# Kernel optimization log

Hardware: AMD Instinct MI355X
Metric: run time of the kernel (lower is better)

## Reference

```python
import jax, jax.numpy as jnp
import numpy as np

B, L, D, F = 1, 4096, 4096, 11008
# (start, end, side): side 0 = vision expert, side 1 = language expert.
# Mirrors merge_section_size over alternating contiguous vision/language token ranges.
SEGMENTS = [(0, 1024, 0), (1024, 2048, 1), (2048, 3072, 0), (3072, 4096, 1)]


def setup_inputs() -> dict:
    key = jax.random.key(0)
    ks = jax.random.split(key, 7)
    s = 0.02  # weight init scale
    hidden_states = jax.random.normal(ks[0], (B, L, D), jnp.float32)
    tt = np.zeros((B, L), np.int32)
    for a, b, side in SEGMENTS:
        tt[:, a:b] = side
    token_type_ids = jnp.asarray(tt)
    lg_w = jax.random.normal(ks[1], (D, F), jnp.float32) * s
    lu_w = jax.random.normal(ks[2], (D, F), jnp.float32) * s
    ld_w = jax.random.normal(ks[3], (F, D), jnp.float32) * s
    vg_w = jax.random.normal(ks[4], (D, F), jnp.float32) * s
    vu_w = jax.random.normal(ks[5], (D, F), jnp.float32) * s
    vd_w = jax.random.normal(ks[6], (F, D), jnp.float32) * s
    return {
        'hidden_states': hidden_states,
        'token_type_ids': token_type_ids,
        'lg_w': lg_w, 'lu_w': lu_w, 'ld_w': ld_w,
        'vg_w': vg_w, 'vu_w': vu_w, 'vd_w': vd_w,
    }


def _swiglu_mlp(x, gw, uw, dw):
    # x: [B, T, D] -> [B, T, D]; down(silu(gate(x)) * up(x))
    h = jax.nn.silu(jnp.einsum('btd,df->btf', x, gw)) * jnp.einsum('btd,df->btf', x, uw)
    return jnp.einsum('btf,fd->btd', h, dw)


def reference(hidden_states, token_type_ids, lg_w, lu_w, ld_w, vg_w, vu_w, vd_w):
    # Split-dispatch over static contiguous segments, then concat along seq dim.
    outs = []
    for a, b, side in SEGMENTS:
        seg = hidden_states[:, a:b, :]
        if side == 1:
            outs.append(_swiglu_mlp(seg, lg_w, lu_w, ld_w))
        else:
            outs.append(_swiglu_mlp(seg, vg_w, vu_w, vd_w))
    return jnp.concatenate(outs, axis=1)
```

## Files before the change

### kernel.cpp

```cpp
#include <hip/hip_runtime.h>
#include <math.h>

typedef unsigned short u16;
typedef short s16x8 __attribute__((ext_vector_type(8)));
typedef float f32x16 __attribute__((ext_vector_type(16)));

#define GLOAD16(gp, lp)                                                        \
  __builtin_amdgcn_global_load_lds(                                            \
      (const __attribute__((address_space(1))) void*)(gp),                     \
      (__attribute__((address_space(3))) void*)(lp), 16, 0, 0)

__device__ __forceinline__ u16 f2bf(float f) {
  union { float f; unsigned u; } v; v.f = f;
  unsigned r = v.u + 0x7fffu + ((v.u >> 16) & 1u);
  return (u16)(r >> 16);
}

__global__ __launch_bounds__(256) void cvt_x_kernel(const float* __restrict__ in,
                                                    u16* __restrict__ out) {
  size_t i = ((size_t)blockIdx.x * 256 + threadIdx.x) * 8;
  float4 a = *(const float4*)(in + i);
  float4 b = *(const float4*)(in + i + 4);
  s16x8 v;
  v[0] = (short)f2bf(a.x); v[1] = (short)f2bf(a.y);
  v[2] = (short)f2bf(a.z); v[3] = (short)f2bf(a.w);
  v[4] = (short)f2bf(b.x); v[5] = (short)f2bf(b.y);
  v[6] = (short)f2bf(b.z); v[7] = (short)f2bf(b.w);
  *(s16x8*)(out + i) = v;
}

__global__ __launch_bounds__(256) void transpose_cvt_kernel(
    const float* __restrict__ in0, const float* __restrict__ in1,
    const float* __restrict__ in2, const float* __restrict__ in3,
    const float* __restrict__ in4, const float* __restrict__ in5,
    u16* __restrict__ o01, u16* __restrict__ o23,
    u16* __restrict__ o4, u16* __restrict__ o5) {
  __shared__ float s[64 * 65];
  const int mat = blockIdx.y;
  const float* in; u16* out;
  switch (mat) {
    case 0: in = in0; out = o01; break;
    case 1: in = in1; out = o01; break;
    case 2: in = in2; out = o23; break;
    case 3: in = in3; out = o23; break;
    case 4: in = in4; out = o4; break;
    default: in = in5; out = o5; break;
  }
  const int R = (mat < 4) ? 4096 : 11008;
  const int C = (mat < 4) ? 11008 : 4096;
  const int nTc = C >> 6;
  const int tr = blockIdx.x / nTc, tc = blockIdx.x - tr * nTc;
  const int r0 = tr << 6, c0 = tc << 6;
  const int t = threadIdx.x;
#pragma unroll
  for (int p = 0; p < 4; ++p) {
    const int lr = p * 16 + (t >> 4);
    const int lc = (t & 15) * 4;
    float4 v = *(const float4*)(in + (size_t)(r0 + lr) * C + (c0 + lc));
    float* sp = &s[lr * 65 + lc];
    sp[0] = v.x; sp[1] = v.y; sp[2] = v.z; sp[3] = v.w;
  }
  __syncthreads();
#pragma unroll
  for (int q = 0; q < 2; ++q) {
    const int oc = q * 32 + (t >> 3);
    const int orr = (t & 7) * 8;
    s16x8 v;
#pragma unroll
    for (int i = 0; i < 8; ++i) v[i] = (short)f2bf(s[(orr + i) * 65 + oc]);
    const int f = c0 + oc;
    size_t orow;
    if (mat < 4) orow = (size_t)((f >> 7) << 8) + ((mat & 1) << 7) + (f & 127);
    else         orow = (size_t)f;
    *(s16x8*)(out + orow * R + (r0 + orr)) = v;
  }
}

#define SBAR() __builtin_amdgcn_s_barrier()
#define LGKM0() asm volatile("s_waitcnt lgkmcnt(0)")
#define LGKM8() asm volatile("s_waitcnt lgkmcnt(8)")
#define VMCNT6() asm volatile("s_waitcnt vmcnt(6)")
#define VMCNT0() asm volatile("s_waitcnt vmcnt(0)")

#define LDA(d, mh)                                                             \
  do {                                                                         \
    _Pragma("unroll") for (int fj = 0; fj < 2; ++fj)                           \
        _Pragma("unroll") for (int ks = 0; ks < 4; ++ks)                       \
        af[fj][ks] = *(const s16x8*)(ldsA + (d) * 32768 + (mh) * 16384 +       \
                                     arow + fj * 4096 + cx[ks]);               \
  } while (0)
#define LDB(d, nh)                                                             \
  do {                                                                         \
    _Pragma("unroll") for (int ks = 0; ks < 4; ++ks)                           \
        bf[nh][ks] = *(const s16x8*)(ldsB + (d) * 32768 + (nh) * 16384 +       \
                                     brow + cx[ks]);                           \
  } while (0)
#define MFMA8(mh, nh)                                                          \
  do {                                                                         \
    __builtin_amdgcn_s_setprio(1);                                             \
    _Pragma("unroll") for (int fj = 0; fj < 2; ++fj)                           \
        _Pragma("unroll") for (int ks = 0; ks < 4; ++ks)                       \
        acc[mh][fj][nh] = __builtin_amdgcn_mfma_f32_32x32x16_bf16(             \
            af[fj][ks], bf[nh][ks], acc[mh][fj][nh], 0, 0, 0);                 \
    __builtin_amdgcn_s_setprio(0);                                             \
  } while (0)

#define STG_A(d, h, kt)                                                        \
  do {                                                                         \
    GLOAD16(srcA + (size_t)((h) * 128) * KB + (size_t)(kt) * 128,              \
            ldsA + (d) * 32768 + (h) * 16384 + woff);                          \
    GLOAD16(srcA + (size_t)((h) * 128 + 64) * KB + (size_t)(kt) * 128,         \
            ldsA + (d) * 32768 + (h) * 16384 + 8192 + woff);                   \
  } while (0)
#define STG_B(d, h, kt)                                                        \
  do {                                                                         \
    GLOAD16(srcB + (size_t)((h) * 128) * KB + (size_t)(kt) * 128,              \
            ldsB + (d) * 32768 + (h) * 16384 + woff);                          \
    GLOAD16(srcB + (size_t)((h) * 128 + 64) * KB + (size_t)(kt) * 128,         \
            ldsB + (d) * 32768 + (h) * 16384 + 8192 + woff);                   \
  } while (0)

#define GEMM_PIPE(NKT)                                                         \
  do {                                                                         \
    STG_A(0, 0, 0); STG_B(0, 0, 0); STG_B(0, 1, 0); STG_A(0, 1, 0);            \
    STG_A(1, 0, 1); STG_B(1, 0, 1); STG_B(1, 1, 1);                            \
    VMCNT6();                                                                  \
    SBAR();                                                                    \
    for (int T = 0; T < (NKT)-2; T += 2) {                                     \
      LDA(0, 0); LDB(0, 0);                                                    \
      STG_A(1, 1, T + 1);                                                      \
      LGKM8();                                                                 \
      SBAR(); LGKM0(); MFMA8(0, 0); SBAR();                                    \
      LDB(0, 1);                                                               \
      STG_A(0, 0, T + 2);                                                      \
      SBAR(); LGKM0(); MFMA8(0, 1); SBAR();                                    \
      LDA(0, 1);                                                               \
      STG_B(0, 0, T + 2);                                                      \
      SBAR(); LGKM0(); MFMA8(1, 1); SBAR();                                    \
      STG_B(0, 1, T + 2);                                                      \
      VMCNT6();                                                                \
      SBAR(); MFMA8(1, 0); SBAR();                                             \
      LDA(1, 0); LDB(1, 0);                                                    \
      STG_A(0, 1, T + 2);                                                      \
      LGKM8();                                                                 \
      SBAR(); LGKM0(); MFMA8(0, 0); SBAR();                                    \
      LDB(1, 1);                                                               \
      STG_A(1, 0, T + 3);                                                      \
      SBAR(); LGKM0(); MFMA8(0, 1); SBAR();                                    \
      LDA(1, 1);                                                               \
      STG_B(1, 0, T + 3);                                                      \
      SBAR(); LGKM0(); MFMA8(1, 1); SBAR();                                    \
      STG_B(1, 1, T + 3);                                                      \
      VMCNT6();                                                                \
      SBAR(); MFMA8(1, 0); SBAR();                                             \
    }                                                                          \
    LDA(0, 0); LDB(0, 0);                                                      \
    STG_A(1, 1, (NKT)-1);                                                      \
    LGKM8();                                                                   \
    SBAR(); LGKM0(); MFMA8(0, 0); SBAR();                                      \
    LDB(0, 1);                                                                 \
    SBAR(); LGKM0(); MFMA8(0, 1); SBAR();                                      \
    LDA(0, 1);                                                                 \
    SBAR(); LGKM0(); MFMA8(1, 1); SBAR();                                      \
    VMCNT0();                                                                  \
    SBAR(); MFMA8(1, 0); SBAR();                                               \
    LDA(1, 0); LDB(1, 0);                                                      \
    LGKM8();                                                                   \
    SBAR(); LGKM0(); MFMA8(0, 0); SBAR();                                      \
    LDB(1, 1);                                                                 \
    SBAR(); LGKM0(); MFMA8(0, 1); SBAR();                                      \
    LDA(1, 1);                                                                 \
    SBAR(); LGKM0(); MFMA8(1, 1); SBAR();                                      \
    MFMA8(1, 0);                                                               \
  } while (0)

__global__ __launch_bounds__(512, 1) void gemm_gateup_persist(
    const u16* __restrict__ A, const u16* __restrict__ GUl,
    const u16* __restrict__ GUv, const int* __restrict__ tt,
    u16* __restrict__ H, int* __restrict__ qcnt) {
  constexpr int KB = 8192;
  __shared__ u16 sA[2][2][128][64];
  __shared__ u16 sB[2][2][128][64];
  __shared__ int sQ;

  const int t = threadIdx.x;
  const int lane = t & 63;
  const int l31 = lane & 31;
  const int kg = lane >> 5;
  const int wn = (t >> 6) & 3;
  const int wm = (t >> 8) & 1;

  const int rowq = t >> 3;
  const int gsw = ((t & 7) ^ (rowq & 7) ^ ((rowq >> 3) & 3)) << 4;
  char* ldsA = (char*)&sA[0][0][0][0];
  char* ldsB = (char*)&sB[0][0][0][0];
  const int woff = (t & 448) << 4;

  const int arow = (wm * 64 + l31) * 128;
  const int brow = (wn * 32 + l31) * 128;
  int cx[4];
#pragma unroll
  for (int ks = 0; ks < 4; ++ks)
    cx[ks] = ((2 * ks + kg) ^ (l31 & 7) ^ ((l31 >> 3) & 3)) << 4;

  for (;;) {
    __syncthreads();
    if (t == 0) sQ = atomicAdd(qcnt, 1);
    __syncthreads();
    const int q = sQ;
    if (q >= 1376) break;
    const int nT = q >> 4;
    const int mT = q & 15;
    const int side = tt[mT << 8];
    const u16* GU = side ? GUl : GUv;
    const char* srcA = (const char*)A + (size_t)(mT * 256 + rowq) * KB + gsw;
    const char* srcB = (const char*)GU + (size_t)(nT * 256 + rowq) * KB + gsw;

    s16x8 af[2][4], bf[2][4];
    f32x16 acc[2][2][2];
#pragma unroll
    for (int a = 0; a < 2; ++a)
#pragma unroll
      for (int b = 0; b < 2; ++b)
#pragma unroll
        for (int c2 = 0; c2 < 2; ++c2)
#pragma unroll
          for (int r = 0; r < 16; ++r) acc[a][b][c2][r] = 0.f;

    GEMM_PIPE(64);

    const int f = nT * 128 + wn * 32 + l31;
#pragma unroll
    for (int mh = 0; mh < 2; ++mh)
#pragma unroll
      for (int fj = 0; fj < 2; ++fj) {
        const int rowbase = mT * 256 + mh * 128 + wm * 64 + fj * 32 + 4 * kg;
#pragma unroll
        for (int r = 0; r < 16; ++r) {
          const int row = rowbase + (r & 3) + 8 * (r >> 2);
          const float gv = acc[mh][fj][0][r];
          const float uv = acc[mh][fj][1][r];
          const float hv = gv / (1.f + __expf(-gv)) * uv;
          H[(size_t)row * 11008 + f] = f2bf(hv);
        }
      }
  }
}

__global__ __launch_bounds__(512, 1) void gemm_down(
    const u16* __restrict__ Hm, const u16* __restrict__ Dl,
    const u16* __restrict__ Dv, const int* __restrict__ tt,
    float* __restrict__ O) {
  constexpr int KB = 22016;
  __shared__ u16 sA[2][2][128][64];
  __shared__ u16 sB[2][2][128][64];

  const int bid = blockIdx.x;
  const int wg = (bid & 7) * 32 + (bid >> 3);
  const int mT = wg & 15;
  const int nT = wg >> 4;

  const int t = threadIdx.x;
  const int lane = t & 63;
  const int l31 = lane & 31;
  const int kg = lane >> 5;
  const int wn = (t >> 6) & 3;
  const int wm = (t >> 8) & 1;

  const int side = tt[mT << 8];
  const u16* B = side ? Dl : Dv;

  const int rowq = t >> 3;
  const int gsw = ((t & 7) ^ (rowq & 7) ^ ((rowq >> 3) & 3)) << 4;
  const char* srcA = (const char*)Hm + (size_t)(mT * 256 + rowq) * KB + gsw;
  const char* srcB = (const char*)B + (size_t)(nT * 256 + rowq) * KB + gsw;
  char* ldsA = (char*)&sA[0][0][0][0];
  char* ldsB = (char*)&sB[0][0][0][0];
  const int woff = (t & 448) << 4;

  const int arow = (wm * 64 + l31) * 128;
  const int brow = (wn * 32 + l31) * 128;
  int cx[4];
#pragma unroll
  for (int ks = 0; ks < 4; ++ks)
    cx[ks] = ((2 * ks + kg) ^ (l31 & 7) ^ ((l31 >> 3) & 3)) << 4;

  s16x8 af[2][4], bf[2][4];
  f32x16 acc[2][2][2];
#pragma unroll
  for (int a = 0; a < 2; ++a)
#pragma unroll
    for (int b = 0; b < 2; ++b)
#pragma unroll
      for (int c2 = 0; c2 < 2; ++c2)
#pragma unroll
        for (int r = 0; r < 16; ++r) acc[a][b][c2][r] = 0.f;

  GEMM_PIPE(172);

#pragma unroll
  for (int mh = 0; mh < 2; ++mh)
#pragma unroll
    for (int fj = 0; fj < 2; ++fj) {
      const int rowbase = mT * 256 + mh * 128 + wm * 64 + fj * 32 + 4 * kg;
#pragma unroll
      for (int nh = 0; nh < 2; ++nh) {
        const int col = nT * 256 + nh * 128 + wn * 32 + l31;
#pragma unroll
        for (int r = 0; r < 16; ++r) {
          const int row = rowbase + (r & 3) + 8 * (r >> 2);
          O[(size_t)row * 4096 + col] = acc[mh][fj][nh][r];
        }
      }
    }
}

extern "C" void kernel_launch(void* const* d_in, const int* in_sizes, int n_in,
                              void* d_out, int out_size, void* d_ws, size_t ws_size,
                              hipStream_t stream) {
  (void)in_sizes; (void)n_in; (void)out_size; (void)ws_size;
  const float* x  = (const float*)d_in[0];
  const int*   tt = (const int*)d_in[1];
  const float* lg = (const float*)d_in[2];
  const float* lu = (const float*)d_in[3];
  const float* ld = (const float*)d_in[4];
  const float* vg = (const float*)d_in[5];
  const float* vu = (const float*)d_in[6];
  const float* vd = (const float*)d_in[7];

  u16* ws  = (u16*)d_ws;
  u16* xbf = ws;
  u16* GUl = xbf + 16777216;
  u16* GUv = GUl + 90177536;
  u16* ldT = GUv + 90177536;
  u16* vdT = ldT + 45088768;
  u16* hbuf = vdT + 45088768;
  int* qcnt = (int*)(hbuf + 45088768);

  hipMemsetAsync(qcnt, 0, 4, stream);
  cvt_x_kernel<<<dim3(8192), dim3(256), 0, stream>>>(x, xbf);
  transpose_cvt_kernel<<<dim3(11008, 6), dim3(256), 0, stream>>>(
      lg, lu, vg, vu, ld, vd, GUl, GUv, ldT, vdT);
  gemm_gateup_persist<<<dim3(256), dim3(512), 0, stream>>>(
      xbf, GUl, GUv, tt, hbuf, qcnt);
  gemm_down<<<dim3(256), dim3(512), 0, stream>>>(hbuf, ldT, vdT, tt, (float*)d_out);
}
```

Before: 1.362 ms.

## Replace atomic work queue with static tile schedule and flattened cross-tile pipeline

The gate/up kernel drops its atomic-counter work queue and assigns each block a fixed M-tile and a strided set of 5 or 6 N-tiles. The K loop runs continuously across those N-tiles, so the next tile's global-to-LDS loads are issued while the current tile finishes, and the SiLU epilogue runs through a hook every 64 steps. The shared pipeline is also rewritten as a single-stage loop with fewer barriers, no partial lgkmcnt waits, and two MFMA groups merged per phase. The goals are to remove per-tile pipeline drain and refill, the atomic and memset overhead, and barrier stalls. In exchange the static 6-vs-5 tile split leaves some blocks with less work, and dropping barriers must not introduce LDS hazards.

Measured after the change: 1.412 ms. +3.6%, slower.

```diff
diff --git a/kernel.cpp b/kernel.cpp
--- a/kernel.cpp
+++ b/kernel.cpp
@@ -78,7 +78,6 @@
 
 #define SBAR() __builtin_amdgcn_s_barrier()
 #define LGKM0() asm volatile("s_waitcnt lgkmcnt(0)")
-#define LGKM8() asm volatile("s_waitcnt lgkmcnt(8)")
 #define VMCNT6() asm volatile("s_waitcnt vmcnt(6)")
 #define VMCNT0() asm volatile("s_waitcnt vmcnt(0)")
 
@@ -105,83 +104,61 @@
     __builtin_amdgcn_s_setprio(0);                                             \
   } while (0)
 
-#define STG_A(d, h, kt)                                                        \
-  do {                                                                         \
-    GLOAD16(srcA + (size_t)((h) * 128) * KB + (size_t)(kt) * 128,              \
-            ldsA + (d) * 32768 + (h) * 16384 + woff);                          \
-    GLOAD16(srcA + (size_t)((h) * 128 + 64) * KB + (size_t)(kt) * 128,         \
-            ldsA + (d) * 32768 + (h) * 16384 + 8192 + woff);                   \
-  } while (0)
-#define STG_B(d, h, kt)                                                        \
-  do {                                                                         \
-    GLOAD16(srcB + (size_t)((h) * 128) * KB + (size_t)(kt) * 128,              \
-            ldsB + (d) * 32768 + (h) * 16384 + woff);                          \
-    GLOAD16(srcB + (size_t)((h) * 128 + 64) * KB + (size_t)(kt) * 128,         \
-            ldsB + (d) * 32768 + (h) * 16384 + 8192 + woff);                   \
-  } while (0)
-
-#define GEMM_PIPE(NKT)                                                         \
+#define GEMM_PIPE3(FKv, HOOK)                                                  \
   do {                                                                         \
     STG_A(0, 0, 0); STG_B(0, 0, 0); STG_B(0, 1, 0); STG_A(0, 1, 0);            \
     STG_A(1, 0, 1); STG_B(1, 0, 1); STG_B(1, 1, 1);                            \
-    VMCNT6();                                                                  \
-    SBAR();                                                                    \
-    for (int T = 0; T < (NKT)-2; T += 2) {                                     \
-      LDA(0, 0); LDB(0, 0);                                                    \
-      STG_A(1, 1, T + 1);                                                      \
-      LGKM8();                                                                 \
-      SBAR(); LGKM0(); MFMA8(0, 0); SBAR();                                    \
-      LDB(0, 1);                                                               \
-      STG_A(0, 0, T + 2);                                                      \
-      SBAR(); LGKM0(); MFMA8(0, 1); SBAR();                                    \
-      LDA(0, 1);                                                               \
-      STG_B(0, 0, T + 2);                                                      \
-      SBAR(); LGKM0(); MFMA8(1, 1); SBAR();                                    \
-      STG_B(0, 1, T + 2);                                                      \
-      VMCNT6();                                                                \
-      SBAR(); MFMA8(1, 0); SBAR();                                             \
-      LDA(1, 0); LDB(1, 0);                                                    \
-      STG_A(0, 1, T + 2);                                                      \
-      LGKM8();                                                                 \
-      SBAR(); LGKM0(); MFMA8(0, 0); SBAR();                                    \
-      LDB(1, 1);                                                               \
-      STG_A(1, 0, T + 3);                                                      \
-      SBAR(); LGKM0(); MFMA8(0, 1); SBAR();                                    \
-      LDA(1, 1);                                                               \
-      STG_B(1, 0, T + 3);                                                      \
-      SBAR(); LGKM0(); MFMA8(1, 1); SBAR();                                    \
-      STG_B(1, 1, T + 3);                                                      \
-      VMCNT6();                                                                \
-      SBAR(); MFMA8(1, 0); SBAR();                                             \
+    VMCNT6(); SBAR();                                                          \
+    for (int T = 0; T < (FKv)-2; ++T) {                                        \
+      const int d = T & 1, nd = d ^ 1;                                         \
+      LDA(d, 0); LDB(d, 0);                                                    \
+      STG_A(nd, 1, T + 1);                                                     \
+      LGKM0(); MFMA8(0, 0); SBAR();                                            \
+      LDB(d, 1);                                                               \
+      STG_A(d, 0, T + 2); STG_B(d, 0, T + 2);                                  \
+      LGKM0(); MFMA8(0, 1); SBAR();                                            \
+      LDA(d, 1);                                                               \
+      STG_B(d, 1, T + 2);                                                      \
+      LGKM0(); MFMA8(1, 1); MFMA8(1, 0);                                       \
+      VMCNT6(); SBAR();                                                        \
+      HOOK;                                                                    \
     }                                                                          \
     LDA(0, 0); LDB(0, 0);                                                      \
-    STG_A(1, 1, (NKT)-1);                                                      \
-    LGKM8();                                                                   \
-    SBAR(); LGKM0(); MFMA8(0, 0); SBAR();                                      \
+    STG_A(1, 1, (FKv)-1);                                                      \
+    LGKM0(); MFMA8(0, 0); SBAR();                                              \
     LDB(0, 1);                                                                 \
-    SBAR(); LGKM0(); MFMA8(0, 1); SBAR();                                      \
+    LGKM0(); MFMA8(0, 1); SBAR();                                              \
     LDA(0, 1);                                                                 \
-    SBAR(); LGKM0(); MFMA8(1, 1); SBAR();                                      \
-    VMCNT0();                                                                  \
-    SBAR(); MFMA8(1, 0); SBAR();                                               \
+    LGKM0(); MFMA8(1, 1); MFMA8(1, 0);                                         \
+    VMCNT0(); SBAR();                                                          \
     LDA(1, 0); LDB(1, 0);                                                      \
-    LGKM8();                                                                   \
-    SBAR(); LGKM0(); MFMA8(0, 0); SBAR();                                      \
+    LGKM0(); MFMA8(0, 0); SBAR();                                              \
     LDB(1, 1);                                                                 \
-    SBAR(); LGKM0(); MFMA8(0, 1); SBAR();                                      \
+    LGKM0(); MFMA8(0, 1); SBAR();                                              \
     LDA(1, 1);                                                                 \
-    SBAR(); LGKM0(); MFMA8(1, 1); SBAR();                                      \
-    MFMA8(1, 0);                                                               \
+    LGKM0(); MFMA8(1, 1); MFMA8(1, 0);                                         \
+  } while (0)
+
+#define ZERO_ACC()                                                             \
+  do {                                                                         \
+    _Pragma("unroll") for (int a = 0; a < 2; ++a)                              \
+        _Pragma("unroll") for (int b = 0; b < 2; ++b)                          \
+        _Pragma("unroll") for (int c2 = 0; c2 < 2; ++c2)                       \
+        _Pragma("unroll") for (int r = 0; r < 16; ++r) acc[a][b][c2][r] = 0.f; \
   } while (0)
 
 __global__ __launch_bounds__(512, 1) void gemm_gateup_persist(
     const u16* __restrict__ A, const u16* __restrict__ GUl,
     const u16* __restrict__ GUv, const int* __restrict__ tt,
-    u16* __restrict__ H, int* __restrict__ qcnt) {
-  constexpr int KB = 8192;
+    u16* __restrict__ H) {
   __shared__ u16 sA[2][2][128][64];
   __shared__ u16 sB[2][2][128][64];
-  __shared__ int sQ;
+
+  const int bid = blockIdx.x;
+  const int c = ((bid >> 7) << 3) | (bid & 7);
+  const int mT = (bid >> 3) & 15;
+  const int ntiles = (c < 6) ? 6 : 5;
+  const int FK = ntiles * 64;
 
   const int t = threadIdx.x;
   const int lane = t & 63;
@@ -190,12 +167,34 @@
   const int wn = (t >> 6) & 3;
   const int wm = (t >> 8) & 1;
 
+  const int side = tt[mT << 8];
+  const u16* GU = side ? GUl : GUv;
+
   const int rowq = t >> 3;
   const int gsw = ((t & 7) ^ (rowq & 7) ^ ((rowq >> 3) & 3)) << 4;
+  const char* srcA = (const char*)A + (size_t)(mT * 256 + rowq) * 8192 + gsw;
+  const char* srcB0 = (const char*)GU + ((size_t)(c * 256) + rowq) * 8192 + gsw;
   char* ldsA = (char*)&sA[0][0][0][0];
   char* ldsB = (char*)&sB[0][0][0][0];
   const int woff = (t & 448) << 4;
 
+#define STG_A(d, h, q)                                                         \
+  do {                                                                         \
+    const char* _pa = srcA + ((q)&63) * 128;                                   \
+    GLOAD16(_pa + (size_t)((h)*128) * 8192,                                    \
+            ldsA + (d)*32768 + (h)*16384 + woff);                              \
+    GLOAD16(_pa + (size_t)((h)*128 + 64) * 8192,                               \
+            ldsA + (d)*32768 + (h)*16384 + 8192 + woff);                       \
+  } while (0)
+#define STG_B(d, h, q)                                                         \
+  do {                                                                         \
+    const char* _pb = srcB0 + (size_t)((q) >> 6) * 33554432 +                  \
+                      (size_t)((h)*128) * 8192 + ((q)&63) * 128;               \
+    GLOAD16(_pb, ldsB + (d)*32768 + (h)*16384 + woff);                         \
+    GLOAD16(_pb + (size_t)64 * 8192,                                           \
+            ldsB + (d)*32768 + (h)*16384 + 8192 + woff);                       \
+  } while (0)
+
   const int arow = (wm * 64 + l31) * 128;
   const int brow = (wn * 32 + l31) * 128;
   int cx[4];
@@ -203,48 +202,32 @@
   for (int ks = 0; ks < 4; ++ks)
     cx[ks] = ((2 * ks + kg) ^ (l31 & 7) ^ ((l31 >> 3) & 3)) << 4;
 
-  for (;;) {
-    __syncthreads();
-    if (t == 0) sQ = atomicAdd(qcnt, 1);
-    __syncthreads();
-    const int q = sQ;
-    if (q >= 1376) break;
-    const int nT = q >> 4;
-    const int mT = q & 15;
-    const int side = tt[mT << 8];
-    const u16* GU = side ? GUl : GUv;
-    const char* srcA = (const char*)A + (size_t)(mT * 256 + rowq) * KB + gsw;
-    const char* srcB = (const char*)GU + (size_t)(nT * 256 + rowq) * KB + gsw;
-
-    s16x8 af[2][4], bf[2][4];
-    f32x16 acc[2][2][2];
-#pragma unroll
-    for (int a = 0; a < 2; ++a)
-#pragma unroll
-      for (int b = 0; b < 2; ++b)
-#pragma unroll
-        for (int c2 = 0; c2 < 2; ++c2)
-#pragma unroll
-          for (int r = 0; r < 16; ++r) acc[a][b][c2][r] = 0.f;
-
-    GEMM_PIPE(64);
-
-    const int f = nT * 128 + wn * 32 + l31;
-#pragma unroll
-    for (int mh = 0; mh < 2; ++mh)
-#pragma unroll
-      for (int fj = 0; fj < 2; ++fj) {
-        const int rowbase = mT * 256 + mh * 128 + wm * 64 + fj * 32 + 4 * kg;
-#pragma unroll
-        for (int r = 0; r < 16; ++r) {
-          const int row = rowbase + (r & 3) + 8 * (r >> 2);
-          const float gv = acc[mh][fj][0][r];
-          const float uv = acc[mh][fj][1][r];
-          const float hv = gv / (1.f + __expf(-gv)) * uv;
-          H[(size_t)row * 11008 + f] = f2bf(hv);
-        }
-      }
-  }
+  s16x8 af[2][4], bf[2][4];
+  f32x16 acc[2][2][2];
+  ZERO_ACC();
+
+#define GU_EPI(nTv)                                                            \
+  do {                                                                         \
+    const int _nT = (nTv);                                                     \
+    const int f = _nT * 128 + wn * 32 + l31;                                   \
+    _Pragma("unroll") for (int mh = 0; mh < 2; ++mh)                           \
+        _Pragma("unroll") for (int fj = 0; fj < 2; ++fj) {                     \
+      const int rowbase = mT * 256 + mh * 128 + wm * 64 + fj * 32 + 4 * kg;    \
+      _Pragma("unroll") for (int r = 0; r < 16; ++r) {                         \
+        const int row = rowbase + (r & 3) + 8 * (r >> 2);                      \
+        const float gv = acc[mh][fj][0][r];                                    \
+        const float uv = acc[mh][fj][1][r];                                    \
+        const float hv = gv / (1.f + __expf(-gv)) * uv;                        \
+        H[(size_t)row * 11008 + f] = f2bf(hv);                                 \
+      }                                                                        \
+    }                                                                          \
+  } while (0)
+
+  GEMM_PIPE3(FK, if ((T & 63) == 63) { GU_EPI(c + 16 * (T >> 6)); ZERO_ACC(); });
+  GU_EPI(c + 16 * (ntiles - 1));
+#undef STG_A
+#undef STG_B
+#undef GU_EPI
 }
 
 __global__ __launch_bounds__(512, 1) void gemm_down(
@@ -278,6 +261,21 @@
   char* ldsB = (char*)&sB[0][0][0][0];
   const int woff = (t & 448) << 4;
 
+#define STG_A(d, h, q)                                                         \
+  do {                                                                         \
+    GLOAD16(srcA + (size_t)((h)*128) * KB + (size_t)(q)*128,                   \
+            ldsA + (d)*32768 + (h)*16384 + woff);                              \
+    GLOAD16(srcA + (size_t)((h)*128 + 64) * KB + (size_t)(q)*128,              \
+            ldsA + (d)*32768 + (h)*16384 + 8192 + woff);                       \
+  } while (0)
+#define STG_B(d, h, q)                                                         \
+  do {                                                                         \
+    GLOAD16(srcB + (size_t)((h)*128) * KB + (size_t)(q)*128,                   \
+            ldsB + (d)*32768 + (h)*16384 + woff);                              \
+    GLOAD16(srcB + (size_t)((h)*128 + 64) * KB + (size_t)(q)*128,              \
+            ldsB + (d)*32768 + (h)*16384 + 8192 + woff);                       \
+  } while (0)
+
   const int arow = (wm * 64 + l31) * 128;
   const int brow = (wn * 32 + l31) * 128;
   int cx[4];
@@ -287,16 +285,9 @@
 
   s16x8 af[2][4], bf[2][4];
   f32x16 acc[2][2][2];
-#pragma unroll
-  for (int a = 0; a < 2; ++a)
-#pragma unroll
-    for (int b = 0; b < 2; ++b)
-#pragma unroll
-      for (int c2 = 0; c2 < 2; ++c2)
-#pragma unroll
-        for (int r = 0; r < 16; ++r) acc[a][b][c2][r] = 0.f;
-
-  GEMM_PIPE(172);
+  ZERO_ACC();
+
+  GEMM_PIPE3(172, ;);
 
 #pragma unroll
   for (int mh = 0; mh < 2; ++mh)
@@ -313,6 +304,8 @@
         }
       }
     }
+#undef STG_A
+#undef STG_B
 }
 
 extern "C" void kernel_launch(void* const* d_in, const int* in_sizes, int n_in,
@@ -335,13 +328,11 @@
   u16* ldT = GUv + 90177536;
   u16* vdT = ldT + 45088768;
   u16* hbuf = vdT + 45088768;
-  int* qcnt = (int*)(hbuf + 45088768);
-
-  hipMemsetAsync(qcnt, 0, 4, stream);
+
   cvt_x_kernel<<<dim3(8192), dim3(256), 0, stream>>>(x, xbf);
   transpose_cvt_kernel<<<dim3(11008, 6), dim3(256), 0, stream>>>(
       lg, lu, vg, vu, ld, vd, GUl, GUv, ldT, vdT);
   gemm_gateup_persist<<<dim3(256), dim3(512), 0, stream>>>(
-      xbf, GUl, GUv, tt, hbuf, qcnt);
+      xbf, GUl, GUv, tt, hbuf);
   gemm_down<<<dim3(256), dim3(512), 0, stream>>>(hbuf, ldT, vdT, tt, (float*)d_out);
 }
```
